# Kernel optimization log

Hardware: AMD Instinct MI355X
Metric: run time of the kernel (lower is better)

Reference implementation:

```python
import jax, jax.numpy as jnp
import numpy as np

H = 16
D_MODEL = 1024
D_K = D_MODEL // H


def setup_inputs() -> dict:
    key = jax.random.key(0)
    ks = jax.random.split(key, 11)
    B, S = 2, 2048
    scale = 1.0 / np.sqrt(D_MODEL)
    inp = {
        "query": jax.random.normal(ks[0], (B, S, D_MODEL), dtype=jnp.float32),
        "key": jax.random.normal(ks[1], (B, S, D_MODEL), dtype=jnp.float32),
        "value": jax.random.normal(ks[2], (B, S, D_MODEL), dtype=jnp.float32),
        "Wq": jax.random.normal(ks[3], (D_MODEL, D_MODEL), dtype=jnp.float32) * scale,
        "bq": jnp.zeros((D_MODEL,), dtype=jnp.float32),
        "Wk": jax.random.normal(ks[4], (D_MODEL, D_MODEL), dtype=jnp.float32) * scale,
        "bk": jnp.zeros((D_MODEL,), dtype=jnp.float32),
        "Wv": jax.random.normal(ks[5], (D_MODEL, D_MODEL), dtype=jnp.float32) * scale,
        "bv": jnp.zeros((D_MODEL,), dtype=jnp.float32),
        "Wo": jax.random.normal(ks[6], (D_MODEL, D_MODEL), dtype=jnp.float32) * scale,
        "bo": jnp.zeros((D_MODEL,), dtype=jnp.float32),
    }
    return inp


def _mha(query, key, value, Wq, bq, Wk, bk, Wv, bv, Wo, bo):
    B, S, _ = query.shape
    # linear projections (torch nn.Linear: x @ W.T + b)
    q = query @ Wq.T + bq
    k = key @ Wk.T + bk
    v = value @ Wv.T + bv
    # split heads: [B, S, D] -> [B, H, S, d_k]
    q = q.reshape(B, S, H, D_K).transpose(0, 2, 1, 3)
    k = k.reshape(B, S, H, D_K).transpose(0, 2, 1, 3)
    v = v.reshape(B, S, H, D_K).transpose(0, 2, 1, 3)
    # scaled dot-product attention with manual stable softmax
    scores = jnp.einsum("bhqd,bhkd->bhqk", q, k) / jnp.sqrt(jnp.float32(D_K))
    stable = scores - jnp.max(scores, axis=-1, keepdims=True)
    e = jnp.exp(stable)
    attn = e / jnp.sum(e, axis=-1, keepdims=True)
    ctx = jnp.einsum("bhqk,bhkd->bhqd", attn, v)
    # merge heads and final projection
    ctx = ctx.transpose(0, 2, 1, 3).reshape(B, S, H * D_K)
    return ctx @ Wo.T + bo


def reference(query, key, value, Wq, bq, Wk, bk, Wv, bv, Wo, bo):
    return _mha(query, key, value, Wq, bq, Wk, bk, Wv, bv, Wo, bo)
```

## Files before the change

### kernel.cpp

```cpp
#include <hip/hip_runtime.h>


#define S_LEN 2048
#define BATCH 2
#define DM    1024
#define NH    16
#define DKH   64
#define BS    (BATCH * S_LEN)

typedef _Float16 f16x8 __attribute__((ext_vector_type(8)));
typedef _Float16 f16x4 __attribute__((ext_vector_type(4)));
typedef _Float16 f16x2 __attribute__((ext_vector_type(2)));
typedef __fp16   h16x2 __attribute__((ext_vector_type(2)));
typedef float    f32x4 __attribute__((ext_vector_type(4)));

__device__ __forceinline__ f16x2 pk_f16(float a, float b) {
  h16x2 r = __builtin_amdgcn_cvt_pkrtz(a, b);
  return __builtin_bit_cast(f16x2, r);
}

__device__ __forceinline__ void gld16(const void* g, void* l) {
  __builtin_amdgcn_global_load_lds(
      (const __attribute__((address_space(1))) void*)g,
      (__attribute__((address_space(3))) void*)l, 16, 0, 0);
}

__device__ __forceinline__ float fast_exp2(float x) {
#if __has_builtin(__builtin_amdgcn_exp2f)
  return __builtin_amdgcn_exp2f(x);
#else
  return exp2f(x);
#endif
}

__global__ __launch_bounds__(256) void cvt_all(
    const float* __restrict__ q, const float* __restrict__ k, const float* __restrict__ v,
    const float* __restrict__ wq, const float* __restrict__ wk,
    const float* __restrict__ wv, const float* __restrict__ wo,
    _Float16* __restrict__ xq, _Float16* __restrict__ xk, _Float16* __restrict__ xv,
    _Float16* __restrict__ w16)
{
  const int y = blockIdx.y;
  const float* src; _Float16* dst; int n;
  if (y == 0)      { src = q;  dst = xq; n = BS * DM; }
  else if (y == 1) { src = k;  dst = xk; n = BS * DM; }
  else if (y == 2) { src = v;  dst = xv; n = BS * DM; }
  else {
    src = (y == 3) ? wq : ((y == 4) ? wk : ((y == 5) ? wv : wo));
    dst = w16 + (size_t)(y - 3) * (DM * DM);
    n = DM * DM;
  }
  int i0 = (blockIdx.x * 256 + threadIdx.x) * 4;
  if (i0 < n) {
    float4 f = *(const float4*)(src + i0);
    f16x2 lo = pk_f16(f.x, f.y);
    f16x2 hi = pk_f16(f.z, f.w);
    f16x4 h; h[0] = lo[0]; h[1] = lo[1]; h[2] = hi[0]; h[3] = hi[1];
    *(f16x4*)(dst + i0) = h;
  }
}

template <typename OUT_T>
__device__ __forceinline__ void gemm_core(
    const _Float16* __restrict__ A, const _Float16* __restrict__ W,
    const float* __restrict__ bias, OUT_T* __restrict__ out, float oscale)
{
  const int tid  = threadIdx.x;
  const int l    = tid & 63;
  const int wv   = tid >> 6;
  const int c    = l & 15, quad = l >> 4;
  const int m0   = blockIdx.y * 128, n0 = blockIdx.x * 128;
  const int wm   = wv & 1, wn = wv >> 1;
  __shared__ _Float16 sA[128 * 64];
  __shared__ _Float16 sB[128 * 64];

  const _Float16* gA[4]; const _Float16* gB[4];
#pragma unroll
  for (int p = 0; p < 4; ++p) {
    int s = tid + p * 256, r = s >> 3, g = (s & 7) ^ (r & 7);
    gA[p] = A + (size_t)(m0 + r) * DM + g * 8;
    gB[p] = W + (size_t)(n0 + r) * DM + g * 8;
  }
  const int cx = c & 7;

  f32x4 acc[4][4] = {};
  for (int k0 = 0; k0 < DM; k0 += 64) {
    __syncthreads();
#pragma unroll
    for (int p = 0; p < 4; ++p) {
      gld16(gA[p] + k0, sA + (tid + p * 256) * 8);
      gld16(gB[p] + k0, sB + (tid + p * 256) * 8);
    }
    __syncthreads();
#pragma unroll
    for (int ks = 0; ks < 2; ++ks) {
      f16x8 af[4], bf[4];
#pragma unroll
      for (int i = 0; i < 4; ++i)
        af[i] = *(const f16x8*)&sA[(wm * 64 + i * 16 + c) * 64 + ((ks * 4 + quad) ^ cx) * 8];
#pragma unroll
      for (int j = 0; j < 4; ++j)
        bf[j] = *(const f16x8*)&sB[(wn * 64 + j * 16 + c) * 64 + ((ks * 4 + quad) ^ cx) * 8];
#pragma unroll
      for (int i = 0; i < 4; ++i)
#pragma unroll
        for (int j = 0; j < 4; ++j)
          acc[i][j] = __builtin_amdgcn_mfma_f32_16x16x32_f16(af[i], bf[j], acc[i][j], 0, 0, 0);
    }
  }
#pragma unroll
  for (int j = 0; j < 4; ++j) {
    int col = n0 + wn * 64 + j * 16 + c;
    float bb = bias[col];
#pragma unroll
    for (int i = 0; i < 4; ++i) {
      int row = m0 + wm * 64 + i * 16 + quad * 4;
#pragma unroll
      for (int r = 0; r < 4; ++r) {
        float vv = (acc[i][j][r] + bb) * oscale;
        out[(size_t)(row + r) * DM + col] = (OUT_T)vv;
      }
    }
  }
}

#define SC_Q (0.125f * 1.44269504088896340736f)

__global__ __launch_bounds__(256) void proj3(
    const _Float16* __restrict__ xq, const _Float16* __restrict__ xk,
    const _Float16* __restrict__ xv, const _Float16* __restrict__ w16,
    const float* __restrict__ bq, const float* __restrict__ bk, const float* __restrict__ bv,
    _Float16* __restrict__ Q, _Float16* __restrict__ K, _Float16* __restrict__ V)
{
  const int z = blockIdx.z;
  const _Float16* A    = (z == 0) ? xq : ((z == 1) ? xk : xv);
  const _Float16* W    = w16 + (size_t)z * (DM * DM);
  const float*    bias = (z == 0) ? bq : ((z == 1) ? bk : bv);
  _Float16*       out  = (z == 0) ? Q : ((z == 1) ? K : V);
  const float     os   = (z == 0) ? SC_Q : 1.0f;
  gemm_core<_Float16>(A, W, bias, out, os);
}

__global__ __launch_bounds__(256) void out_gemm(
    const _Float16* __restrict__ ctx, const _Float16* __restrict__ wo,
    const float* __restrict__ bo, float* __restrict__ out)
{
  gemm_core<float>(ctx, wo, bo, out, 1.0f);
}

__global__ __launch_bounds__(256) void vtrans(const _Float16* __restrict__ V,
                                              _Float16* __restrict__ Vt)
{
  const int tid = threadIdx.x;
  const int s0  = blockIdx.x * 64;
  const int bh  = blockIdx.y;
  const int b   = bh >> 4, h = bh & 15;
  __shared__ _Float16 t[64 * 68];
  const _Float16* Vg = V + ((size_t)(b * S_LEN + s0)) * DM + h * DKH;
#pragma unroll
  for (int p = 0; p < 2; ++p) {
    int cc = tid + p * 256;
    int r = cc >> 3, off = (cc & 7) << 3;
    f16x8 vv = *(const f16x8*)(Vg + (size_t)r * DM + off);
    f16x4 lo, hi;
    lo.x = vv[0]; lo.y = vv[1]; lo.z = vv[2]; lo.w = vv[3];
    hi.x = vv[4]; hi.y = vv[5]; hi.z = vv[6]; hi.w = vv[7];
    *(f16x4*)&t[r * 68 + off]     = lo;
    *(f16x4*)&t[r * 68 + off + 4] = hi;
  }
  __syncthreads();
  const int cpos = tid & 63, dbase = tid >> 6;
  _Float16* Og = Vt + ((size_t)bh * DKH) * S_LEN + s0 + cpos;
#pragma unroll
  for (int i = 0; i < 16; ++i) {
    int d = dbase + i * 4;
    Og[(size_t)d * S_LEN] = t[cpos * 68 + d];
  }
}

#define APP 72
__global__ __launch_bounds__(256) void attn(
    const _Float16* __restrict__ Q, const _Float16* __restrict__ K,
    const _Float16* __restrict__ Vt, _Float16* __restrict__ ctx)
{
  const int tid = threadIdx.x;
  const int l   = tid & 63, wv = tid >> 6;
  const int c   = l & 15, quad = l >> 4;
  const int q0  = blockIdx.x * 128;
  const int bh  = blockIdx.y;
  const int b   = bh >> 4, h = bh & 15;
  __shared__ _Float16 sK[64 * 64];
  __shared__ _Float16 sV[64 * 64];
  __shared__ _Float16 sP[4][32 * APP];

  f16x8 qf[2][2];
#pragma unroll
  for (int qc = 0; qc < 2; ++qc) {
    const _Float16* Qg = Q + ((size_t)(b * S_LEN + q0 + wv * 32 + qc * 16 + c)) * DM + h * DKH;
    qf[qc][0] = *(const f16x8*)(Qg + quad * 8);
    qf[qc][1] = *(const f16x8*)(Qg + 32 + quad * 8);
  }

  f32x4 o[2][4] = {};
  float l_part[2] = {};

  const _Float16* Kg0 = K + ((size_t)b * S_LEN) * DM + h * DKH;
  const _Float16* Vg0 = Vt + ((size_t)bh * DKH) * S_LEN;

  const int sa = tid,      ra = sa >> 3, ba = (sa & 7) ^ (ra & 7);
  const int sb = tid + 256, rb = sb >> 3, bb = (sb & 7) ^ (rb & 7);
  const _Float16* gKa = Kg0 + (size_t)ra * DM + ba * 8;
  const _Float16* gKb = Kg0 + (size_t)rb * DM + bb * 8;
  const _Float16* gVa = Vg0 + (size_t)ra * S_LEN + ba * 8;
  const _Float16* gVb = Vg0 + (size_t)rb * S_LEN + bb * 8;
  const int cx = c & 7;

  for (int kt = 0; kt < S_LEN / 64; ++kt) {
    const int k0 = kt * 64;
    __syncthreads();
    gld16(gKa + (size_t)k0 * DM, sK + sa * 8);
    gld16(gKb + (size_t)k0 * DM, sK + sb * 8);
    gld16(gVa + k0,              sV + sa * 8);
    gld16(gVb + k0,              sV + sb * 8);
    __syncthreads();

    f32x4 sAcc[2][4] = {};
#pragma unroll
    for (int ks = 0; ks < 2; ++ks)
#pragma unroll
      for (int nt = 0; nt < 4; ++nt) {
        f16x8 kf = *(const f16x8*)&sK[(nt * 16 + c) * 64 + ((ks * 4 + quad) ^ cx) * 8];
#pragma unroll
        for (int qc = 0; qc < 2; ++qc)
          sAcc[qc][nt] = __builtin_amdgcn_mfma_f32_16x16x32_f16(kf, qf[qc][ks], sAcc[qc][nt], 0, 0, 0);
      }

#pragma unroll
    for (int qc = 0; qc < 2; ++qc)
#pragma unroll
      for (int nt = 0; nt < 4; ++nt) {
        float p0 = fast_exp2(sAcc[qc][nt][0]);
        float p1 = fast_exp2(sAcc[qc][nt][1]);
        float p2 = fast_exp2(sAcc[qc][nt][2]);
        float p3 = fast_exp2(sAcc[qc][nt][3]);
        l_part[qc] += (p0 + p1) + (p2 + p3);
        f16x2 lo = pk_f16(p0, p1);
        f16x2 hi = pk_f16(p2, p3);
        f16x4 pk; pk[0] = lo[0]; pk[1] = lo[1]; pk[2] = hi[0]; pk[3] = hi[1];
        *(f16x4*)&sP[wv][(qc * 16 + c) * APP + nt * 16 + quad * 4] = pk;
      }

#pragma unroll
    for (int ks = 0; ks < 2; ++ks) {
      f16x8 bf[4];
#pragma unroll
      for (int nt = 0; nt < 4; ++nt)
        bf[nt] = *(const f16x8*)&sV[(nt * 16 + c) * 64 + ((ks * 4 + quad) ^ cx) * 8];
#pragma unroll
      for (int qc = 0; qc < 2; ++qc) {
        f16x8 af = *(const f16x8*)&sP[wv][(qc * 16 + c) * APP + ks * 32 + quad * 8];
#pragma unroll
        for (int nt = 0; nt < 4; ++nt)
          o[qc][nt] = __builtin_amdgcn_mfma_f32_16x16x32_f16(af, bf[nt], o[qc][nt], 0, 0, 0);
      }
    }
  }

#pragma unroll
  for (int qc = 0; qc < 2; ++qc) {
    float lp = l_part[qc];
    lp += __shfl_xor(lp, 16);
    lp += __shfl_xor(lp, 32);
    _Float16* Og = ctx + ((size_t)(b * S_LEN + q0 + wv * 32 + qc * 16 + quad * 4)) * DM + h * DKH;
#pragma unroll
    for (int j = 0; j < 4; ++j) {
      float s = __shfl(lp, quad * 4 + j, 64);
      float inv = 1.0f / s;
#pragma unroll
      for (int nt = 0; nt < 4; ++nt)
        Og[(size_t)j * DM + nt * 16 + c] = (_Float16)(o[qc][nt][j] * inv);
    }
  }
}

extern "C" void kernel_launch(void* const* d_in, const int* in_sizes, int n_in,
                              void* d_out, int out_size, void* d_ws, size_t ws_size,
                              hipStream_t stream)
{
  (void)in_sizes; (void)n_in; (void)out_size; (void)ws_size;
  const float* q  = (const float*)d_in[0];
  const float* k  = (const float*)d_in[1];
  const float* v  = (const float*)d_in[2];
  const float* wq = (const float*)d_in[3];
  const float* bq = (const float*)d_in[4];
  const float* wk = (const float*)d_in[5];
  const float* bk = (const float*)d_in[6];
  const float* wv = (const float*)d_in[7];
  const float* bv = (const float*)d_in[8];
  const float* wo = (const float*)d_in[9];
  const float* bo = (const float*)d_in[10];

  char* ws = (char*)d_ws;
  _Float16* XQ  = (_Float16*)(ws);
  _Float16* XK  = (_Float16*)(ws + (8u  << 20));
  _Float16* XV  = (_Float16*)(ws + (16u << 20));
  _Float16* W16 = (_Float16*)(ws + (24u << 20));
  _Float16* Qp  = (_Float16*)(ws + (32u << 20));
  _Float16* Kp  = (_Float16*)(ws + (40u << 20));
  _Float16* Vp  = (_Float16*)(ws + (48u << 20));
  _Float16* VT  = XK;
  _Float16* CTX = XQ;
  float* out = (float*)d_out;

  cvt_all<<<dim3(4096, 7), 256, 0, stream>>>(q, k, v, wq, wk, wv, wo, XQ, XK, XV, W16);
  proj3<<<dim3(8, 32, 3), 256, 0, stream>>>(XQ, XK, XV, W16, bq, bk, bv, Qp, Kp, Vp);
  vtrans<<<dim3(32, 32), 256, 0, stream>>>(Vp, VT);
  attn<<<dim3(16, 32), 256, 0, stream>>>(Qp, Kp, VT, CTX);
  out_gemm<<<dim3(8, 32), 256, 0, stream>>>(CTX, W16 + (size_t)3 * DM * DM, bo, out);
}
```

Baseline: 251.6 us.

## Fuse V transpose into projection epilogue and retile attention across query/dim waves

The V projection GEMM epilogue now writes V directly in head-transposed [b,h,d,s] layout with 4-wide fp16 stores, which removes the separate vtrans kernel and its extra global round trip. The attention kernel is retiled: each block handles 64 queries instead of 128, so the grid doubles. Each wave computes scores for 16 keys across all 64 queries, then shares P through LDS. The PV product is split across waves by query half and head-dim half, and row sums are reduced through shared memory. This adds a block-wide barrier per key tile and halves the reuse of each K/V tile per block, in exchange for more blocks and a smaller per-wave register footprint.

```diff
diff --git a/kernel.cpp b/kernel.cpp
--- a/kernel.cpp
+++ b/kernel.cpp
@@ -60,7 +60,7 @@
   }
 }
 
-template <typename OUT_T>
+template <typename OUT_T, bool VT>
 __device__ __forceinline__ void gemm_core(
     const _Float16* __restrict__ A, const _Float16* __restrict__ W,
     const float* __restrict__ bias, OUT_T* __restrict__ out, float oscale)
@@ -108,17 +108,36 @@
           acc[i][j] = __builtin_amdgcn_mfma_f32_16x16x32_f16(af[i], bf[j], acc[i][j], 0, 0, 0);
     }
   }
-#pragma unroll
-  for (int j = 0; j < 4; ++j) {
-    int col = n0 + wn * 64 + j * 16 + c;
-    float bb = bias[col];
-#pragma unroll
-    for (int i = 0; i < 4; ++i) {
-      int row = m0 + wm * 64 + i * 16 + quad * 4;
-#pragma unroll
-      for (int r = 0; r < 4; ++r) {
-        float vv = (acc[i][j][r] + bb) * oscale;
-        out[(size_t)(row + r) * DM + col] = (OUT_T)vv;
+  if constexpr (VT) {
+#pragma unroll
+    for (int j = 0; j < 4; ++j) {
+      int col = n0 + wn * 64 + j * 16 + c;
+      float bb = bias[col];
+      int hh = col >> 6, dd = col & 63;
+#pragma unroll
+      for (int i = 0; i < 4; ++i) {
+        int row = m0 + wm * 64 + i * 16 + quad * 4;
+        int bb2 = row >> 11, ss = row & (S_LEN - 1);
+        _Float16* dst = (_Float16*)out + ((size_t)(bb2 * NH + hh) * DKH + dd) * S_LEN + ss;
+        f16x4 v4;
+#pragma unroll
+        for (int r = 0; r < 4; ++r) v4[r] = (_Float16)((acc[i][j][r] + bb) * oscale);
+        *(f16x4*)dst = v4;
+      }
+    }
+  } else {
+#pragma unroll
+    for (int j = 0; j < 4; ++j) {
+      int col = n0 + wn * 64 + j * 16 + c;
+      float bb = bias[col];
+#pragma unroll
+      for (int i = 0; i < 4; ++i) {
+        int row = m0 + wm * 64 + i * 16 + quad * 4;
+#pragma unroll
+        for (int r = 0; r < 4; ++r) {
+          float vv = (acc[i][j][r] + bb) * oscale;
+          out[(size_t)(row + r) * DM + col] = (OUT_T)vv;
+        }
       }
     }
   }
@@ -130,52 +149,23 @@
     const _Float16* __restrict__ xq, const _Float16* __restrict__ xk,
     const _Float16* __restrict__ xv, const _Float16* __restrict__ w16,
     const float* __restrict__ bq, const float* __restrict__ bk, const float* __restrict__ bv,
-    _Float16* __restrict__ Q, _Float16* __restrict__ K, _Float16* __restrict__ V)
+    _Float16* __restrict__ Q, _Float16* __restrict__ K, _Float16* __restrict__ Vt)
 {
   const int z = blockIdx.z;
-  const _Float16* A    = (z == 0) ? xq : ((z == 1) ? xk : xv);
-  const _Float16* W    = w16 + (size_t)z * (DM * DM);
-  const float*    bias = (z == 0) ? bq : ((z == 1) ? bk : bv);
-  _Float16*       out  = (z == 0) ? Q : ((z == 1) ? K : V);
-  const float     os   = (z == 0) ? SC_Q : 1.0f;
-  gemm_core<_Float16>(A, W, bias, out, os);
+  if (z == 2) {
+    gemm_core<_Float16, true>(xv, w16 + (size_t)2 * DM * DM, bv, Vt, 1.0f);
+  } else if (z == 0) {
+    gemm_core<_Float16, false>(xq, w16, bq, Q, SC_Q);
+  } else {
+    gemm_core<_Float16, false>(xk, w16 + (size_t)DM * DM, bk, K, 1.0f);
+  }
 }
 
 __global__ __launch_bounds__(256) void out_gemm(
     const _Float16* __restrict__ ctx, const _Float16* __restrict__ wo,
     const float* __restrict__ bo, float* __restrict__ out)
 {
-  gemm_core<float>(ctx, wo, bo, out, 1.0f);
-}
-
-__global__ __launch_bounds__(256) void vtrans(const _Float16* __restrict__ V,
-                                              _Float16* __restrict__ Vt)
-{
-  const int tid = threadIdx.x;
-  const int s0  = blockIdx.x * 64;
-  const int bh  = blockIdx.y;
-  const int b   = bh >> 4, h = bh & 15;
-  __shared__ _Float16 t[64 * 68];
-  const _Float16* Vg = V + ((size_t)(b * S_LEN + s0)) * DM + h * DKH;
-#pragma unroll
-  for (int p = 0; p < 2; ++p) {
-    int cc = tid + p * 256;
-    int r = cc >> 3, off = (cc & 7) << 3;
-    f16x8 vv = *(const f16x8*)(Vg + (size_t)r * DM + off);
-    f16x4 lo, hi;
-    lo.x = vv[0]; lo.y = vv[1]; lo.z = vv[2]; lo.w = vv[3];
-    hi.x = vv[4]; hi.y = vv[5]; hi.z = vv[6]; hi.w = vv[7];
-    *(f16x4*)&t[r * 68 + off]     = lo;
-    *(f16x4*)&t[r * 68 + off + 4] = hi;
-  }
-  __syncthreads();
-  const int cpos = tid & 63, dbase = tid >> 6;
-  _Float16* Og = Vt + ((size_t)bh * DKH) * S_LEN + s0 + cpos;
-#pragma unroll
-  for (int i = 0; i < 16; ++i) {
-    int d = dbase + i * 4;
-    Og[(size_t)d * S_LEN] = t[cpos * 68 + d];
-  }
+  gemm_core<float, false>(ctx, wo, bo, out, 1.0f);
 }
 
 #define APP 72
@@ -186,28 +176,30 @@
   const int tid = threadIdx.x;
   const int l   = tid & 63, wv = tid >> 6;
   const int c   = l & 15, quad = l >> 4;
-  const int q0  = blockIdx.x * 128;
+  const int q0  = blockIdx.x * 64;
   const int bh  = blockIdx.y;
   const int b   = bh >> 4, h = bh & 15;
+  const int wq  = wv & 1, wd = wv >> 1;
   __shared__ _Float16 sK[64 * 64];
   __shared__ _Float16 sV[64 * 64];
-  __shared__ _Float16 sP[4][32 * APP];
-
-  f16x8 qf[2][2];
-#pragma unroll
-  for (int qc = 0; qc < 2; ++qc) {
-    const _Float16* Qg = Q + ((size_t)(b * S_LEN + q0 + wv * 32 + qc * 16 + c)) * DM + h * DKH;
-    qf[qc][0] = *(const f16x8*)(Qg + quad * 8);
-    qf[qc][1] = *(const f16x8*)(Qg + 32 + quad * 8);
-  }
-
-  f32x4 o[2][4] = {};
-  float l_part[2] = {};
+  __shared__ _Float16 sP[64 * APP];
+  __shared__ float    lsum[64][4];
+
+  f16x8 qf[4][2];
+#pragma unroll
+  for (int nt = 0; nt < 4; ++nt) {
+    const _Float16* Qg = Q + ((size_t)(b * S_LEN + q0 + nt * 16 + c)) * DM + h * DKH;
+    qf[nt][0] = *(const f16x8*)(Qg + quad * 8);
+    qf[nt][1] = *(const f16x8*)(Qg + 32 + quad * 8);
+  }
+
+  f32x4 o[2][2] = {};
+  float l_part[4] = {};
 
   const _Float16* Kg0 = K + ((size_t)b * S_LEN) * DM + h * DKH;
   const _Float16* Vg0 = Vt + ((size_t)bh * DKH) * S_LEN;
 
-  const int sa = tid,      ra = sa >> 3, ba = (sa & 7) ^ (ra & 7);
+  const int sa = tid,       ra = sa >> 3, ba = (sa & 7) ^ (ra & 7);
   const int sb = tid + 256, rb = sb >> 3, bb = (sb & 7) ^ (rb & 7);
   const _Float16* gKa = Kg0 + (size_t)ra * DM + ba * 8;
   const _Float16* gKb = Kg0 + (size_t)rb * DM + bb * 8;
@@ -224,61 +216,70 @@
     gld16(gVb + k0,              sV + sb * 8);
     __syncthreads();
 
-    f32x4 sAcc[2][4] = {};
-#pragma unroll
-    for (int ks = 0; ks < 2; ++ks)
-#pragma unroll
-      for (int nt = 0; nt < 4; ++nt) {
-        f16x8 kf = *(const f16x8*)&sK[(nt * 16 + c) * 64 + ((ks * 4 + quad) ^ cx) * 8];
-#pragma unroll
-        for (int qc = 0; qc < 2; ++qc)
-          sAcc[qc][nt] = __builtin_amdgcn_mfma_f32_16x16x32_f16(kf, qf[qc][ks], sAcc[qc][nt], 0, 0, 0);
-      }
-
-#pragma unroll
-    for (int qc = 0; qc < 2; ++qc)
-#pragma unroll
-      for (int nt = 0; nt < 4; ++nt) {
-        float p0 = fast_exp2(sAcc[qc][nt][0]);
-        float p1 = fast_exp2(sAcc[qc][nt][1]);
-        float p2 = fast_exp2(sAcc[qc][nt][2]);
-        float p3 = fast_exp2(sAcc[qc][nt][3]);
-        l_part[qc] += (p0 + p1) + (p2 + p3);
-        f16x2 lo = pk_f16(p0, p1);
-        f16x2 hi = pk_f16(p2, p3);
-        f16x4 pk; pk[0] = lo[0]; pk[1] = lo[1]; pk[2] = hi[0]; pk[3] = hi[1];
-        *(f16x4*)&sP[wv][(qc * 16 + c) * APP + nt * 16 + quad * 4] = pk;
-      }
-
+    f32x4 sAcc[4] = {};
 #pragma unroll
     for (int ks = 0; ks < 2; ++ks) {
-      f16x8 bf[4];
+      f16x8 kf = *(const f16x8*)&sK[(wv * 16 + c) * 64 + ((ks * 4 + quad) ^ cx) * 8];
 #pragma unroll
       for (int nt = 0; nt < 4; ++nt)
-        bf[nt] = *(const f16x8*)&sV[(nt * 16 + c) * 64 + ((ks * 4 + quad) ^ cx) * 8];
-#pragma unroll
-      for (int qc = 0; qc < 2; ++qc) {
-        f16x8 af = *(const f16x8*)&sP[wv][(qc * 16 + c) * APP + ks * 32 + quad * 8];
-#pragma unroll
-        for (int nt = 0; nt < 4; ++nt)
-          o[qc][nt] = __builtin_amdgcn_mfma_f32_16x16x32_f16(af, bf[nt], o[qc][nt], 0, 0, 0);
-      }
-    }
-  }
-
-#pragma unroll
-  for (int qc = 0; qc < 2; ++qc) {
-    float lp = l_part[qc];
-    lp += __shfl_xor(lp, 16);
-    lp += __shfl_xor(lp, 32);
-    _Float16* Og = ctx + ((size_t)(b * S_LEN + q0 + wv * 32 + qc * 16 + quad * 4)) * DM + h * DKH;
-#pragma unroll
-    for (int j = 0; j < 4; ++j) {
-      float s = __shfl(lp, quad * 4 + j, 64);
-      float inv = 1.0f / s;
-#pragma unroll
-      for (int nt = 0; nt < 4; ++nt)
-        Og[(size_t)j * DM + nt * 16 + c] = (_Float16)(o[qc][nt][j] * inv);
+        sAcc[nt] = __builtin_amdgcn_mfma_f32_16x16x32_f16(kf, qf[nt][ks], sAcc[nt], 0, 0, 0);
+    }
+
+#pragma unroll
+    for (int nt = 0; nt < 4; ++nt) {
+      float p0 = fast_exp2(sAcc[nt][0]);
+      float p1 = fast_exp2(sAcc[nt][1]);
+      float p2 = fast_exp2(sAcc[nt][2]);
+      float p3 = fast_exp2(sAcc[nt][3]);
+      l_part[nt] += (p0 + p1) + (p2 + p3);
+      f16x2 lo = pk_f16(p0, p1);
+      f16x2 hi = pk_f16(p2, p3);
+      f16x4 pk; pk[0] = lo[0]; pk[1] = lo[1]; pk[2] = hi[0]; pk[3] = hi[1];
+      *(f16x4*)&sP[(nt * 16 + c) * APP + wv * 16 + quad * 4] = pk;
+    }
+    __syncthreads();
+
+#pragma unroll
+    for (int ks = 0; ks < 2; ++ks) {
+      f16x8 af[2], bf[2];
+#pragma unroll
+      for (int qb = 0; qb < 2; ++qb)
+        af[qb] = *(const f16x8*)&sP[(wq * 32 + qb * 16 + c) * APP + ks * 32 + quad * 8];
+#pragma unroll
+      for (int db = 0; db < 2; ++db)
+        bf[db] = *(const f16x8*)&sV[(wd * 32 + db * 16 + c) * 64 + ((ks * 4 + quad) ^ cx) * 8];
+#pragma unroll
+      for (int qb = 0; qb < 2; ++qb)
+#pragma unroll
+        for (int db = 0; db < 2; ++db)
+          o[qb][db] = __builtin_amdgcn_mfma_f32_16x16x32_f16(af[qb], bf[db], o[qb][db], 0, 0, 0);
+    }
+  }
+
+#pragma unroll
+  for (int nt = 0; nt < 4; ++nt) {
+    float s = l_part[nt];
+    s += __shfl_xor(s, 16);
+    s += __shfl_xor(s, 32);
+    l_part[nt] = s;
+  }
+  if (quad == 0) {
+#pragma unroll
+    for (int nt = 0; nt < 4; ++nt) lsum[nt * 16 + c][wv] = l_part[nt];
+  }
+  __syncthreads();
+
+#pragma unroll
+  for (int qb = 0; qb < 2; ++qb) {
+#pragma unroll
+    for (int r = 0; r < 4; ++r) {
+      int q = wq * 32 + qb * 16 + quad * 4 + r;
+      f32x4 ls = *(const f32x4*)&lsum[q][0];
+      float inv = 1.0f / (ls[0] + ls[1] + ls[2] + ls[3]);
+      _Float16* Og = ctx + ((size_t)(b * S_LEN + q0 + q)) * DM + h * DKH;
+#pragma unroll
+      for (int db = 0; db < 2; ++db)
+        Og[wd * 32 + db * 16 + c] = (_Float16)(o[qb][db][r] * inv);
     }
   }
 }
@@ -307,14 +308,12 @@
   _Float16* W16 = (_Float16*)(ws + (24u << 20));
   _Float16* Qp  = (_Float16*)(ws + (32u << 20));
   _Float16* Kp  = (_Float16*)(ws + (40u << 20));
-  _Float16* Vp  = (_Float16*)(ws + (48u << 20));
-  _Float16* VT  = XK;
+  _Float16* VT  = (_Float16*)(ws + (48u << 20));
   _Float16* CTX = XQ;
   float* out = (float*)d_out;
 
   cvt_all<<<dim3(4096, 7), 256, 0, stream>>>(q, k, v, wq, wk, wv, wo, XQ, XK, XV, W16);
-  proj3<<<dim3(8, 32, 3), 256, 0, stream>>>(XQ, XK, XV, W16, bq, bk, bv, Qp, Kp, Vp);
-  vtrans<<<dim3(32, 32), 256, 0, stream>>>(Vp, VT);
-  attn<<<dim3(16, 32), 256, 0, stream>>>(Qp, Kp, VT, CTX);
+  proj3<<<dim3(8, 32, 3), 256, 0, stream>>>(XQ, XK, XV, W16, bq, bk, bv, Qp, Kp, VT);
+  attn<<<dim3(32, 32), 256, 0, stream>>>(Qp, Kp, VT, CTX);
   out_gemm<<<dim3(8, 32), 256, 0, stream>>>(CTX, W16 + (size_t)3 * DM * DM, bo, out);
 }
```

New measurement: 240.1 us. 1.05x faster.
